# Kernel optimization log

Hardware: AMD Instinct MI355X
Metric: run time of the kernel (lower is better)

Reference implementation:

```python
import jax, jax.numpy as jnp
import numpy as np

TOP_K = 2  # num_expert in the torch module


def setup_inputs() -> dict:
    key = jax.random.key(0)
    ks = jax.random.split(key, 8)
    B, C, H, W, E, Dh = 8, 512, 32, 32, 8, 1024
    inputs = jax.random.normal(ks[0], (B, C, H, W), dtype=jnp.float32)
    k = jax.random.uniform(ks[1], (B, 1, 1, 1), dtype=jnp.float32)
    # gate: global-avg-pool + Linear(C -> E)
    Wg = jax.random.normal(ks[2], (C, E), dtype=jnp.float32) / np.sqrt(C)
    bg = jnp.zeros((E,), dtype=jnp.float32)
    # experts: per-expert 2-layer channel MLP (1x1-conv style), modulated by k
    W1 = jax.random.normal(ks[3], (E, C, Dh), dtype=jnp.float32) / np.sqrt(C)
    b1 = jnp.zeros((E, Dh), dtype=jnp.float32)
    W2 = jax.random.normal(ks[4], (E, Dh, C), dtype=jnp.float32) / np.sqrt(Dh)
    b2 = jnp.zeros((E, C), dtype=jnp.float32)
    return {"inputs": inputs, "k": k, "Wg": Wg, "bg": bg,
            "W1": W1, "b1": b1, "W2": W2, "b2": b2}


def reference(inputs, k, Wg, bg, W1, b1, W2, b2):
    B = inputs.shape[0]
    # --- gate: softmax in fp32, cast back (matches F.softmax(dtype=torch.float)) ---
    logits = jnp.mean(inputs, axis=(2, 3)) @ Wg + bg            # [B, E]
    weights = jax.nn.softmax(logits.astype(jnp.float32), axis=1).astype(inputs.dtype)
    topk_w, topk_idx = jax.lax.top_k(weights, TOP_K)            # [B, K]
    # --- scatter top-k gate weights into dense [B, E] mask (training path) ---
    exp_w = jnp.zeros_like(weights).at[jnp.arange(B)[:, None], topk_idx].set(topk_w)
    # --- run ALL experts densely (training-mode math), masked combine ---
    h = jnp.einsum('bchw,ecd->bedhw', inputs, W1) + b1[None, :, :, None, None]
    h = jax.nn.gelu(h, approximate=False)                        # [B,E,Dh,H,W]
    y = jnp.einsum('bedhw,edc->bechw', h, W2) + b2[None, :, :, None, None]
    y = y * k[:, None]                                           # per-sample scalar mod
    out = inputs + jnp.einsum('bechw,be->bchw', y, exp_w)        # residual + weighted sum
    return out
```

## Files before the change

kernel.cpp:

```cpp
#include <hip/hip_runtime.h>
#include <hip/hip_bf16.h>
#include <math.h>


typedef __bf16 bf16_t;
typedef __attribute__((ext_vector_type(8))) __bf16 bf16x8;
typedef __attribute__((ext_vector_type(4))) __bf16 bf16x4;
typedef __attribute__((ext_vector_type(4))) float f32x4;

#define GLDS(g, l) __builtin_amdgcn_global_load_lds(                      \
    (const __attribute__((address_space(1))) void*)(const void*)(g),       \
    (__attribute__((address_space(3))) void*)(void*)(l), 16, 0, 0)

__device__ __forceinline__ float gelu_fast(float x) {
    float z = x * 0.70710678118654752f;
    float az = fabsf(z);
    float t = 1.0f / (1.0f + 0.3275911f * az);
    float p = ((((1.061405429f * t - 1.453152027f) * t + 1.421413741f) * t
                - 0.284496736f) * t + 0.254829592f) * t;
    float e = __expf(-az * az);
    float er = copysignf(1.0f - p * e, z);
    return 0.5f * x * (1.0f + er);
}

__global__ __launch_bounds__(256) void transpose_cvt_all(
    const float* __restrict__ x, const float* __restrict__ W1,
    const float* __restrict__ W2, bf16_t* __restrict__ xT,
    bf16_t* __restrict__ W1t, bf16_t* __restrict__ W2t, float* __restrict__ pp) {
    int id = blockIdx.x;
    const float* src; bf16_t* dst; int Rows, Cols, csh; bool dm = false;
    if (id < 1024)      { src = x;  dst = xT;  Rows = 512;  Cols = 1024; csh = 4; dm = true; }
    else if (id < 2048) { id -= 1024; src = W1; dst = W1t; Rows = 512;  Cols = 1024; csh = 4; }
    else                { id -= 2048; src = W2; dst = W2t; Rows = 1024; Cols = 512; csh = 3; }
    const int bz = id >> 7, t = id & 127;
    const int ct = t & ((1 << csh) - 1), rt = t >> csh;
    const int r0 = rt * 64, c0 = ct * 64;
    __shared__ float tile[64][65];
    const int tid = threadIdx.x;
    const int lrw = tid >> 4, lcol = (tid & 15) * 4;
    const float* sb = src + (size_t)bz * Rows * Cols + c0;
    #pragma unroll
    for (int p = 0; p < 4; ++p) {
        const int row = p * 16 + lrw;
        float4 v = *(const float4*)(sb + (size_t)(r0 + row) * Cols + lcol);
        tile[row][lcol + 0] = v.x; tile[row][lcol + 1] = v.y;
        tile[row][lcol + 2] = v.z; tile[row][lcol + 3] = v.w;
    }
    __syncthreads();
    if (dm) {
        const int row = tid >> 2, q = tid & 3;
        float s = 0.f;
        #pragma unroll
        for (int j = 0; j < 16; ++j) s += tile[row][q * 16 + j];
        s += __shfl_down(s, 2, 4);
        s += __shfl_down(s, 1, 4);
        if (q == 0) pp[(bz * 16 + ct) * 512 + r0 + row] = s;
    }
    bf16_t* db = dst + (size_t)bz * Rows * Cols + r0;
    #pragma unroll
    for (int q = 0; q < 2; ++q) {
        const int idq = q * 256 + tid;
        const int orow = idq >> 3, seg = idq & 7;
        bf16_t ov[8];
        #pragma unroll
        for (int j = 0; j < 8; ++j) ov[j] = (bf16_t)tile[seg * 8 + j][orow];
        *(bf16x8*)(db + (size_t)(c0 + orow) * Rows + seg * 8) = *(bf16x8*)ov;
    }
}

__global__ void gate_kernel(const float* __restrict__ pp, const float* __restrict__ Wg,
                            const float* __restrict__ bg, const float* __restrict__ kmod,
                            int* __restrict__ tidx, float* __restrict__ scale) {
    const int tid = threadIdx.x;
    const int b = tid >> 6, l = tid & 63;
    float a[8] = {0.f, 0.f, 0.f, 0.f, 0.f, 0.f, 0.f, 0.f};
    for (int c = l; c < 512; c += 64) {
        float m = 0.f;
        #pragma unroll
        for (int ht = 0; ht < 16; ++ht) m += pp[(b * 16 + ht) * 512 + c];
        #pragma unroll
        for (int e = 0; e < 8; ++e) a[e] += m * Wg[c * 8 + e];
    }
    #pragma unroll
    for (int e = 0; e < 8; ++e)
        #pragma unroll
        for (int off = 32; off; off >>= 1) a[e] += __shfl_xor(a[e], off, 64);
    if (l == 0) {
        float lg[8], mx = -1e30f;
        #pragma unroll
        for (int e = 0; e < 8; ++e) { lg[e] = a[e] * (1.0f / 1024.0f) + bg[e]; mx = fmaxf(mx, lg[e]); }
        float sum = 0.f;
        #pragma unroll
        for (int e = 0; e < 8; ++e) { lg[e] = expf(lg[e] - mx); sum += lg[e]; }
        float inv = 1.0f / sum;
        float best = -1.f; int i0 = 0;
        for (int j = 0; j < 8; ++j) { float w = lg[j] * inv; if (w > best) { best = w; i0 = j; } }
        float best2 = -1.f; int i1 = 0;
        for (int j = 0; j < 8; ++j) { if (j == i0) continue; float w = lg[j] * inv; if (w > best2) { best2 = w; i1 = j; } }
        float kb = kmod[b];
        tidx[b * 2] = i0; tidx[b * 2 + 1] = i1;
        scale[b * 2] = best * kb; scale[b * 2 + 1] = best2 * kb;
    }
}

__global__ __launch_bounds__(256, 4) void gemm1_kernel(
    const bf16_t* __restrict__ W1t, const bf16_t* __restrict__ xT,
    const float* __restrict__ b1, const int* __restrict__ tidx,
    const float* __restrict__ scale, bf16_t* __restrict__ hT) {
    __shared__ bf16_t smem[17408];
    const int bid = blockIdx.x;
    const int pair = bid >> 6, rem = bid & 63;
    const int b = pair >> 1, slot = pair & 1;
    const int e = tidx[pair];
    const float s = scale[pair];
    const int d0 = (rem >> 3) * 128, n0 = (rem & 7) * 128;
    const int tid = threadIdx.x;
    const int lane = tid & 63, wave = tid >> 6;
    const int wm = (wave & 1) * 64, wn = (wave >> 1) * 64;
    const int lrow = lane & 15, quad = lane >> 4;

    const bf16_t* gA = W1t + (size_t)e * 524288 + (size_t)d0 * 512;
    const bf16_t* gB = xT + (size_t)b * 524288 + (size_t)n0 * 512;

    f32x4 acc[4][4];
    #pragma unroll
    for (int i = 0; i < 4; ++i)
        #pragma unroll
        for (int j = 0; j < 4; ++j) acc[i][j] = (f32x4){0.f, 0.f, 0.f, 0.f};

    for (int it = 0; it < 8; ++it) {
        const int k0 = it * 64;
        #pragma unroll
        for (int p = 0; p < 4; ++p) {
            const int row = p * 32 + (tid >> 3);
            const int cg = ((tid & 7) ^ (row & 7)) * 8;
            GLDS(gA + (size_t)row * 512 + k0 + cg, smem + (p * 256 + tid) * 8);
            GLDS(gB + (size_t)row * 512 + k0 + cg, smem + 8192 + (p * 256 + tid) * 8);
        }
        __syncthreads();
        #pragma unroll
        for (int kh = 0; kh < 2; ++kh) {
            const int swz = ((kh * 4 + quad) ^ (lrow & 7)) * 8;
            bf16x8 af[4], bfr[4];
            #pragma unroll
            for (int i = 0; i < 4; ++i) {
                af[i]  = *(const bf16x8*)&smem[(wm + i * 16 + lrow) * 64 + swz];
                bfr[i] = *(const bf16x8*)&smem[8192 + (wn + i * 16 + lrow) * 64 + swz];
            }
            #pragma unroll
            for (int i = 0; i < 4; ++i)
                #pragma unroll
                for (int j = 0; j < 4; ++j)
                    acc[i][j] = __builtin_amdgcn_mfma_f32_16x16x32_bf16(af[i], bfr[j], acc[i][j], 0, 0, 0);
        }
        __syncthreads();
    }

    bf16_t* hTb = hT + (size_t)b * 2097152 + slot * 1024;
    #pragma unroll
    for (int i = 0; i < 4; ++i) {
        const int d_l = wm + i * 16 + quad * 4;
        const float4 bb = *(const float4*)(b1 + e * 1024 + d0 + d_l);
        #pragma unroll
        for (int j = 0; j < 4; ++j) {
            const int hw_l = wn + j * 16 + lrow;
            f32x4 a = acc[i][j];
            bf16x4 o = { (bf16_t)(gelu_fast(a[0] + bb.x) * s),
                         (bf16_t)(gelu_fast(a[1] + bb.y) * s),
                         (bf16_t)(gelu_fast(a[2] + bb.z) * s),
                         (bf16_t)(gelu_fast(a[3] + bb.w) * s) };
            *(bf16x4*)&smem[hw_l * 136 + d_l] = o;
        }
    }
    __syncthreads();
    #pragma unroll
    for (int q = 0; q < 8; ++q) {
        const int idx = q * 256 + tid;
        const int row = idx >> 4, c16 = idx & 15;
        bf16x8 v = *(const bf16x8*)&smem[row * 136 + c16 * 8];
        *(bf16x8*)(hTb + (size_t)(n0 + row) * 2048 + d0 + c16 * 8) = v;
    }
}

__global__ __launch_bounds__(256, 2) void gemm2_kernel(
    const bf16_t* __restrict__ W2t, const bf16_t* __restrict__ hT,
    const float* __restrict__ b2, const int* __restrict__ tidx,
    const float* __restrict__ scale, const float* __restrict__ x,
    float* __restrict__ out) {
    __shared__ bf16_t smem[24576];
    const int bid = blockIdx.x;
    const int b = bid >> 6, rem = bid & 63;
    const int c0 = (rem >> 3) * 64, hw0 = (rem & 7) * 128;
    const int e0 = tidx[b * 2], e1 = tidx[b * 2 + 1];
    const float s0 = scale[b * 2], s1 = scale[b * 2 + 1];
    const int tid = threadIdx.x;
    const int lane = tid & 63, wave = tid >> 6;
    const int wm = (wave & 1) * 64;
    const int wc = (wave >> 1) * 32;
    const int lrow = lane & 15, quad = lane >> 4;

    const bf16_t* hTb = hT + (size_t)b * 2097152 + (size_t)hw0 * 2048;
    const bf16_t* B0 = W2t + (size_t)e0 * 524288 + (size_t)c0 * 1024;
    const bf16_t* B1 = W2t + (size_t)e1 * 524288 + (size_t)c0 * 1024;

    f32x4 acc[4][2];
    #pragma unroll
    for (int i = 0; i < 4; ++i)
        #pragma unroll
        for (int j = 0; j < 2; ++j) acc[i][j] = (f32x4){0.f, 0.f, 0.f, 0.f};

    auto stage = [&](int st, int it) {
        const int k0 = it * 64;
        bf16_t* dst = smem + st * 12288;
        #pragma unroll
        for (int p = 0; p < 4; ++p) {
            const int row = p * 32 + (tid >> 3);
            const int cg = ((tid & 7) ^ (row & 7)) * 8;
            GLDS(hTb + (size_t)row * 2048 + k0 + cg, dst + (p * 256 + tid) * 8);
        }
        const bf16_t* gB = ((it < 16) ? B0 : B1) + (k0 & 1023);
        #pragma unroll
        for (int p = 0; p < 2; ++p) {
            const int row = p * 32 + (tid >> 3);
            const int cg = ((tid & 7) ^ (row & 7)) * 8;
            GLDS(gB + (size_t)row * 1024 + cg, dst + 8192 + (p * 256 + tid) * 8);
        }
    };

    stage(0, 0);
    __syncthreads();

    for (int it = 0; it < 32; ++it) {
        const int cur = it & 1;
        if (it < 31) stage(cur ^ 1, it + 1);
        const bf16_t* cA = smem + cur * 12288;
        const bf16_t* cB = cA + 8192;
        #pragma unroll
        for (int kh = 0; kh < 2; ++kh) {
            const int swz = ((kh * 4 + quad) ^ (lrow & 7)) * 8;
            bf16x8 af[4], bfr[2];
            #pragma unroll
            for (int i = 0; i < 4; ++i)
                af[i] = *(const bf16x8*)&cA[(wm + i * 16 + lrow) * 64 + swz];
            #pragma unroll
            for (int j = 0; j < 2; ++j)
                bfr[j] = *(const bf16x8*)&cB[(wc + j * 16 + lrow) * 64 + swz];
            #pragma unroll
            for (int i = 0; i < 4; ++i)
                #pragma unroll
                for (int j = 0; j < 2; ++j)
                    acc[i][j] = __builtin_amdgcn_mfma_f32_16x16x32_bf16(af[i], bfr[j], acc[i][j], 0, 0, 0);
        }
        __syncthreads();
    }

    #pragma unroll
    for (int j = 0; j < 2; ++j) {
        const int c = c0 + wc + j * 16 + lrow;
        const float bias = s0 * b2[e0 * 512 + c] + s1 * b2[e1 * 512 + c];
        #pragma unroll
        for (int i = 0; i < 4; ++i) {
            const int hw = hw0 + wm + i * 16 + quad * 4;
            const size_t o = ((size_t)(b * 512 + c)) * 1024 + hw;
            const float4 xv = *(const float4*)(x + o);
            float4 ov = { acc[i][j][0] + xv.x + bias, acc[i][j][1] + xv.y + bias,
                          acc[i][j][2] + xv.z + bias, acc[i][j][3] + xv.w + bias };
            *(float4*)(out + o) = ov;
        }
    }
}

extern "C" void kernel_launch(void* const* d_in, const int* in_sizes, int n_in,
                              void* d_out, int out_size, void* d_ws, size_t ws_size,
                              hipStream_t stream) {
    const float* x    = (const float*)d_in[0];
    const float* kmod = (const float*)d_in[1];
    const float* Wg   = (const float*)d_in[2];
    const float* bg   = (const float*)d_in[3];
    const float* W1   = (const float*)d_in[4];
    const float* b1   = (const float*)d_in[5];
    const float* W2   = (const float*)d_in[6];
    const float* b2   = (const float*)d_in[7];
    float* out = (float*)d_out;

    char* ws = (char*)d_ws;
    int*   tix  = (int*)ws;
    float* scl  = (float*)(ws + 64);
    bf16_t* xT  = (bf16_t*)(ws + 32768);
    bf16_t* W1t = (bf16_t*)(ws + 32768 + (size_t)8388608);
    bf16_t* W2t = (bf16_t*)(ws + 32768 + (size_t)2 * 8388608);
    bf16_t* hT  = (bf16_t*)(ws + 32768 + (size_t)3 * 8388608);
    float* pp   = (float*)hT;

    transpose_cvt_all<<<3072, 256, 0, stream>>>(x, W1, W2, xT, W1t, W2t, pp);
    gate_kernel<<<1, 512, 0, stream>>>(pp, Wg, bg, kmod, tix, scl);
    gemm1_kernel<<<1024, 256, 0, stream>>>(W1t, xT, b1, tix, scl, hT);
    gemm2_kernel<<<512, 256, 0, stream>>>(W2t, hT, b2, tix, scl, x, out);
}
```

Before: 174.9 us.

## Double-buffer gemm1 with larger 128x256 tiles and interleave block-to-pair mapping

Gemm1 now computes a 128x256 output tile per block (half as many blocks), with K-step 32 and a two-stage LDS double buffer so global loads of the next slice overlap MFMA work on the current one. The epilogue writes its output in two 128-row chunks through shared memory. Block indices in both GEMMs are remapped so consecutive blocks span different batch/expert pairs, which spreads work across experts and may change L2 locality. The larger accumulator (128 floats per thread) raises register pressure and launch bounds drop to 2 blocks per CU, lowering occupancy.

```diff
diff --git a/kernel.cpp b/kernel.cpp
--- a/kernel.cpp
+++ b/kernel.cpp
@@ -103,82 +103,104 @@
     }
 }
 
-__global__ __launch_bounds__(256, 4) void gemm1_kernel(
+__global__ __launch_bounds__(256, 2) void gemm1_kernel(
     const bf16_t* __restrict__ W1t, const bf16_t* __restrict__ xT,
     const float* __restrict__ b1, const int* __restrict__ tidx,
     const float* __restrict__ scale, bf16_t* __restrict__ hT) {
-    __shared__ bf16_t smem[17408];
+    __shared__ bf16_t smem[24576];
     const int bid = blockIdx.x;
-    const int pair = bid >> 6, rem = bid & 63;
+    const int pair = bid & 15, tile = bid >> 4;
     const int b = pair >> 1, slot = pair & 1;
     const int e = tidx[pair];
     const float s = scale[pair];
-    const int d0 = (rem >> 3) * 128, n0 = (rem & 7) * 128;
+    const int d0 = (tile & 7) * 128, hw0 = (tile >> 3) * 256;
     const int tid = threadIdx.x;
     const int lane = tid & 63, wave = tid >> 6;
-    const int wm = (wave & 1) * 64, wn = (wave >> 1) * 64;
+    const int wm = (wave & 1) * 64, wn = (wave >> 1) * 128;
     const int lrow = lane & 15, quad = lane >> 4;
 
     const bf16_t* gA = W1t + (size_t)e * 524288 + (size_t)d0 * 512;
-    const bf16_t* gB = xT + (size_t)b * 524288 + (size_t)n0 * 512;
-
-    f32x4 acc[4][4];
+    const bf16_t* gB = xT + (size_t)b * 524288 + (size_t)hw0 * 512;
+
+    f32x4 acc[4][8];
     #pragma unroll
     for (int i = 0; i < 4; ++i)
         #pragma unroll
-        for (int j = 0; j < 4; ++j) acc[i][j] = (f32x4){0.f, 0.f, 0.f, 0.f};
-
-    for (int it = 0; it < 8; ++it) {
-        const int k0 = it * 64;
+        for (int j = 0; j < 8; ++j) acc[i][j] = (f32x4){0.f, 0.f, 0.f, 0.f};
+
+    auto stage = [&](int st, int k0) {
+        bf16_t* dA = smem + st * 12288;
+        bf16_t* dB = dA + 4096;
+        #pragma unroll
+        for (int p = 0; p < 2; ++p) {
+            const int sl = p * 256 + tid;
+            const int row = sl >> 2, cg = ((sl & 3) ^ (row & 3)) * 8;
+            GLDS(gA + (size_t)row * 512 + k0 + cg, dA + sl * 8);
+        }
         #pragma unroll
         for (int p = 0; p < 4; ++p) {
-            const int row = p * 32 + (tid >> 3);
-            const int cg = ((tid & 7) ^ (row & 7)) * 8;
-            GLDS(gA + (size_t)row * 512 + k0 + cg, smem + (p * 256 + tid) * 8);
-            GLDS(gB + (size_t)row * 512 + k0 + cg, smem + 8192 + (p * 256 + tid) * 8);
-        }
+            const int sl = p * 256 + tid;
+            const int row = sl >> 2, cg = ((sl & 3) ^ (row & 3)) * 8;
+            GLDS(gB + (size_t)row * 512 + k0 + cg, dB + sl * 8);
+        }
+    };
+
+    stage(0, 0);
+    __syncthreads();
+
+    for (int it = 0; it < 16; ++it) {
+        const int cur = it & 1;
+        if (it < 15) stage(cur ^ 1, (it + 1) * 32);
+        const bf16_t* cA = smem + cur * 12288;
+        const bf16_t* cB = cA + 4096;
+        const int swz = (quad ^ (lrow & 3)) * 8;
+        bf16x8 af[4], bfr[8];
+        #pragma unroll
+        for (int i = 0; i < 4; ++i)
+            af[i] = *(const bf16x8*)&cA[(wm + i * 16 + lrow) * 32 + swz];
+        #pragma unroll
+        for (int j = 0; j < 8; ++j)
+            bfr[j] = *(const bf16x8*)&cB[(wn + j * 16 + lrow) * 32 + swz];
+        #pragma unroll
+        for (int i = 0; i < 4; ++i)
+            #pragma unroll
+            for (int j = 0; j < 8; ++j)
+                acc[i][j] = __builtin_amdgcn_mfma_f32_16x16x32_bf16(af[i], bfr[j], acc[i][j], 0, 0, 0);
         __syncthreads();
-        #pragma unroll
-        for (int kh = 0; kh < 2; ++kh) {
-            const int swz = ((kh * 4 + quad) ^ (lrow & 7)) * 8;
-            bf16x8 af[4], bfr[4];
-            #pragma unroll
-            for (int i = 0; i < 4; ++i) {
-                af[i]  = *(const bf16x8*)&smem[(wm + i * 16 + lrow) * 64 + swz];
-                bfr[i] = *(const bf16x8*)&smem[8192 + (wn + i * 16 + lrow) * 64 + swz];
-            }
+    }
+
+    bf16_t* hTb = hT + (size_t)b * 2097152 + slot * 1024;
+    float4 bb[4];
+    #pragma unroll
+    for (int i = 0; i < 4; ++i)
+        bb[i] = *(const float4*)(b1 + e * 1024 + d0 + wm + i * 16 + quad * 4);
+
+    #pragma unroll
+    for (int chk = 0; chk < 2; ++chk) {
+        if (wn == chk * 128) {
             #pragma unroll
             for (int i = 0; i < 4; ++i)
                 #pragma unroll
-                for (int j = 0; j < 4; ++j)
-                    acc[i][j] = __builtin_amdgcn_mfma_f32_16x16x32_bf16(af[i], bfr[j], acc[i][j], 0, 0, 0);
+                for (int j = 0; j < 8; ++j) {
+                    const int hw_l = j * 16 + lrow;
+                    const int d_l = wm + i * 16 + quad * 4;
+                    f32x4 a = acc[i][j];
+                    bf16x4 o = { (bf16_t)(gelu_fast(a[0] + bb[i].x) * s),
+                                 (bf16_t)(gelu_fast(a[1] + bb[i].y) * s),
+                                 (bf16_t)(gelu_fast(a[2] + bb[i].z) * s),
+                                 (bf16_t)(gelu_fast(a[3] + bb[i].w) * s) };
+                    *(bf16x4*)&smem[hw_l * 136 + d_l] = o;
+                }
         }
         __syncthreads();
-    }
-
-    bf16_t* hTb = hT + (size_t)b * 2097152 + slot * 1024;
-    #pragma unroll
-    for (int i = 0; i < 4; ++i) {
-        const int d_l = wm + i * 16 + quad * 4;
-        const float4 bb = *(const float4*)(b1 + e * 1024 + d0 + d_l);
-        #pragma unroll
-        for (int j = 0; j < 4; ++j) {
-            const int hw_l = wn + j * 16 + lrow;
-            f32x4 a = acc[i][j];
-            bf16x4 o = { (bf16_t)(gelu_fast(a[0] + bb.x) * s),
-                         (bf16_t)(gelu_fast(a[1] + bb.y) * s),
-                         (bf16_t)(gelu_fast(a[2] + bb.z) * s),
-                         (bf16_t)(gelu_fast(a[3] + bb.w) * s) };
-            *(bf16x4*)&smem[hw_l * 136 + d_l] = o;
-        }
-    }
-    __syncthreads();
-    #pragma unroll
-    for (int q = 0; q < 8; ++q) {
-        const int idx = q * 256 + tid;
-        const int row = idx >> 4, c16 = idx & 15;
-        bf16x8 v = *(const bf16x8*)&smem[row * 136 + c16 * 8];
-        *(bf16x8*)(hTb + (size_t)(n0 + row) * 2048 + d0 + c16 * 8) = v;
+        #pragma unroll
+        for (int q = 0; q < 8; ++q) {
+            const int idx = q * 256 + tid;
+            const int row = idx >> 4, seg = idx & 15;
+            bf16x8 v = *(const bf16x8*)&smem[row * 136 + seg * 8];
+            *(bf16x8*)(hTb + (size_t)(hw0 + chk * 128 + row) * 2048 + d0 + seg * 8) = v;
+        }
+        __syncthreads();
     }
 }
 
@@ -189,7 +211,7 @@
     float* __restrict__ out) {
     __shared__ bf16_t smem[24576];
     const int bid = blockIdx.x;
-    const int b = bid >> 6, rem = bid & 63;
+    const int b = bid & 7, rem = bid >> 3;
     const int c0 = (rem >> 3) * 64, hw0 = (rem & 7) * 128;
     const int e0 = tidx[b * 2], e1 = tidx[b * 2 + 1];
     const float s0 = scale[b * 2], s1 = scale[b * 2 + 1];
@@ -294,6 +316,6 @@
 
     transpose_cvt_all<<<3072, 256, 0, stream>>>(x, W1, W2, xT, W1t, W2t, pp);
     gate_kernel<<<1, 512, 0, stream>>>(pp, Wg, bg, kmod, tix, scl);
-    gemm1_kernel<<<1024, 256, 0, stream>>>(W1t, xT, b1, tix, scl, hT);
+    gemm1_kernel<<<512, 256, 0, stream>>>(W1t, xT, b1, tix, scl, hT);
     gemm2_kernel<<<512, 256, 0, stream>>>(W2t, hT, b2, tix, scl, x, out);
 }
```

After: 184.6 us. 5.5% more time.
